# Performance work log

Measured on AMD Instinct MI355X. Metric: run time of the kernel, lower is better.

Reference implementation:

```python
import jax, jax.numpy as jnp
import numpy as np

N = 10000   # nodes (cells)
E = 100000  # edges
G = 2000    # num_genes
H = 20      # heads
C1 = 128    # layer-1 out channels per head
C2 = 128    # latent_dim
NEG_SLOPE = 0.2


def setup_inputs():
    key = jax.random.key(0)
    ks = jax.random.split(key, 9)
    s = 0.05
    return {
        "x": jax.random.normal(ks[0], (N, G), jnp.float32),
        "edge_index": jax.random.randint(ks[1], (2, E), 0, N, dtype=jnp.int64),
        "W1": jax.random.normal(ks[2], (G, H * C1), jnp.float32) * s,
        "att_src1": jax.random.normal(ks[3], (H, C1), jnp.float32) * s,
        "att_dst1": jax.random.normal(ks[4], (H, C1), jnp.float32) * s,
        "b1": jnp.zeros((H * C1,), jnp.float32),
        "W2": jax.random.normal(ks[5], (H * C1, H * C2), jnp.float32) * s,
        "att_src2": jax.random.normal(ks[6], (H, C2), jnp.float32) * s,
        "att_dst2": jax.random.normal(ks[7], (H, C2), jnp.float32) * s,
        "b2": jnp.zeros((C2,), jnp.float32),
    }


def _gat_conv(x, W, att_src, att_dst, bias, src, dst, concat):
    """PyG GATConv (eval mode, self-loops already in src/dst)."""
    n = x.shape[0]
    h_, c_ = att_src.shape
    h = (x @ W).reshape(n, h_, c_)                      # [N, H, C]
    a_src = jnp.einsum("nhc,hc->nh", h, att_src)        # [N, H]
    a_dst = jnp.einsum("nhc,hc->nh", h, att_dst)        # [N, H]
    e = a_src[src] + a_dst[dst]                          # [E, H]
    e = jnp.where(e > 0, e, NEG_SLOPE * e)               # leaky_relu
    # segment softmax over incoming edges of each destination node
    e_max = jax.ops.segment_max(e, dst, num_segments=n)  # [N, H]
    ex = jnp.exp(e - e_max[dst])                         # [E, H]
    denom = jax.ops.segment_sum(ex, dst, num_segments=n)
    alpha = ex / denom[dst]                              # [E, H]
    msg = alpha[:, :, None] * h[src]                     # [E, H, C]
    out = jax.ops.segment_sum(msg, dst, num_segments=n)  # [N, H, C]
    if concat:
        out = out.reshape(n, h_ * c_)
    else:
        out = out.mean(axis=1)                           # [N, C]
    return out + bias


def reference(x, edge_index, W1, att_src1, att_dst1, b1, W2, att_src2, att_dst2, b2):
    n = x.shape[0]
    loop = jnp.arange(n, dtype=edge_index.dtype)
    src = jnp.concatenate([edge_index[0], loop])  # PyG add_self_loops=True
    dst = jnp.concatenate([edge_index[1], loop])
    h1 = _gat_conv(x, W1, att_src1, att_dst1, b1, src, dst, concat=True)
    h1 = jax.nn.relu(h1)  # dropout is identity in eval mode
    h2 = _gat_conv(h1, W2, att_src2, att_dst2, b2, src, dst, concat=False)
    return jax.nn.relu(h2)
```

## Files before the change

### kernel.cpp

```cpp
#include <hip/hip_runtime.h>

#define NEG_SLOPE 0.2f

typedef __attribute__((ext_vector_type(4))) float floatx4;
typedef __attribute__((ext_vector_type(8))) short shortx8;

__device__ __forceinline__ unsigned short f2bf(float f) {
  union { float f; unsigned int u; } v;
  v.f = f;
  unsigned int r = (v.u + 0x7FFFu + ((v.u >> 16) & 1u)) >> 16;
  return (unsigned short)r;
}
__device__ __forceinline__ float bf2f(unsigned short u) {
  union { unsigned int u; float f; } v;
  v.u = (unsigned int)u << 16;
  return v.f;
}
__device__ __forceinline__ void store_out(float* p, float v) { *p = v; }
__device__ __forceinline__ void store_out(unsigned short* p, float v) { *p = f2bf(v); }

__device__ __forceinline__ void gload_lds16(const unsigned short* g, unsigned short* l) {
  __builtin_amdgcn_global_load_lds(
      (const __attribute__((address_space(1))) void*)(g),
      (__attribute__((address_space(3))) void*)(l), 16, 0, 0);
}

__device__ __forceinline__ int load_edge(const void* ei, long idx, int is64) {
  if (is64) return (int)((const long long*)ei)[idx];
  return ((const int*)ei)[idx];
}

__global__ void detect64_kernel(const unsigned int* __restrict__ p, int* __restrict__ flag) {
  int is64 = 1;
  for (int i = 0; i < 32; ++i)
    if (p[2 * i + 1] != 0u) is64 = 0;
  *flag = is64;
}

__global__ void init_cnt_kernel(int* __restrict__ cnt, int n) {
  int i = blockIdx.x * blockDim.x + threadIdx.x;
  if (i < n) cnt[i] = 1;
}

__global__ void count_kernel(const void* __restrict__ ei, const int* __restrict__ flag, int E,
                             int* __restrict__ cnt) {
  int e = blockIdx.x * blockDim.x + threadIdx.x;
  if (e >= E) return;
  int is64 = *flag;
  int d = load_edge(ei, (long)E + e, is64);
  atomicAdd(&cnt[d], 1);
}

__global__ __launch_bounds__(1024) void scan_kernel(const int* __restrict__ cnt,
                                                    int* __restrict__ offs, int n) {
  __shared__ int partial[1024];
  int t = threadIdx.x;
  int per = (n + 1023) / 1024;
  int beg = t * per;
  int end = min(beg + per, n);
  int sum = 0;
  for (int i = beg; i < end; ++i) sum += cnt[i];
  partial[t] = sum;
  __syncthreads();
  for (int d = 1; d < 1024; d <<= 1) {
    int v = (t >= d) ? partial[t - d] : 0;
    __syncthreads();
    partial[t] += v;
    __syncthreads();
  }
  int excl = (t == 0) ? 0 : partial[t - 1];
  for (int i = beg; i < end; ++i) { offs[i] = excl; excl += cnt[i]; }
  if (t == 1023) offs[n] = partial[1023];
}

__global__ void init_self_kernel(const int* __restrict__ offs, int* __restrict__ srcs,
                                 int* __restrict__ fill, int n) {
  int i = blockIdx.x * blockDim.x + threadIdx.x;
  if (i < n) { srcs[offs[i]] = i; fill[i] = 1; }
}

__global__ void scatter_kernel(const void* __restrict__ ei, const int* __restrict__ flag, int E,
                               const int* __restrict__ offs, int* __restrict__ fill,
                               int* __restrict__ srcs) {
  int e = blockIdx.x * blockDim.x + threadIdx.x;
  if (e >= E) return;
  int is64 = *flag;
  int s = load_edge(ei, e, is64);
  int d = load_edge(ei, (long)E + e, is64);
  int pos = offs[d] + atomicAdd(&fill[d], 1);
  srcs[pos] = s;
}


__global__ __launch_bounds__(256) void pack_a_kernel(const float* __restrict__ in,
                                                     unsigned short* __restrict__ out, int M,
                                                     int K, int Kpad) {
  int rt = blockIdx.x;
  int r = threadIdx.x & 127;
  int kq = threadIdx.x >> 7;
  int row = rt * 128 + r;
  int nkc = Kpad >> 3;
  unsigned short* obase = out + (long)rt * Kpad * 128 + r * 8;
  const float* irow = in + (long)row * K;
  for (int kc = kq + (int)blockIdx.y * 2; kc < nkc; kc += (int)gridDim.y * 2) {
    int k = kc << 3;
    shortx8 o;
    if (row < M && k + 8 <= K && (K & 3) == 0) {
      float4 v0 = *(const float4*)(irow + k);
      float4 v1 = *(const float4*)(irow + k + 4);
      o[0] = (short)f2bf(v0.x); o[1] = (short)f2bf(v0.y);
      o[2] = (short)f2bf(v0.z); o[3] = (short)f2bf(v0.w);
      o[4] = (short)f2bf(v1.x); o[5] = (short)f2bf(v1.y);
      o[6] = (short)f2bf(v1.z); o[7] = (short)f2bf(v1.w);
    } else {
#pragma unroll
      for (int i = 0; i < 8; ++i) {
        int kk = k + i;
        float v = (row < M && kk < K) ? irow[kk] : 0.f;
        o[i] = (short)f2bf(v);
      }
    }
    *(shortx8*)(obase + (long)kc * 1024) = o;
  }
}

__global__ __launch_bounds__(256) void transpose_pack_kernel(const float* __restrict__ in,
                                                             unsigned short* __restrict__ out,
                                                             int K, int N, int Kpad) {
  __shared__ float tile[32][33];
  int kb = blockIdx.x * 32;
  int nb = blockIdx.y * 32;
  int tx = threadIdx.x & 31;
  int ty = threadIdx.x >> 5;
#pragma unroll
  for (int i = 0; i < 32; i += 8) {
    int k = kb + ty + i;
    tile[ty + i][tx] = (k < K) ? in[(long)k * N + nb + tx] : 0.f;
  }
  __syncthreads();
  if (threadIdx.x < 128) {
    int nl = threadIdx.x & 31;
    int nn = nb + nl;
    int kc4 = threadIdx.x >> 5;
    int k0 = kc4 * 8;
    shortx8 o;
#pragma unroll
    for (int j = 0; j < 8; ++j) o[j] = (short)f2bf(tile[k0 + j][nl]);
    int kc = (kb >> 3) + kc4;
    *(shortx8*)(out + (long)(nn >> 7) * Kpad * 128 + (long)kc * 1024 + (nn & 127) * 8) = o;
  }
}

template <typename OT>
__global__ __launch_bounds__(256) void mfma_gemm_kernel(const unsigned short* __restrict__ A,
                                                        const unsigned short* __restrict__ Bt,
                                                        OT* __restrict__ C,
                                                        const float* __restrict__ att_s,
                                                        const float* __restrict__ att_d,
                                                        float* __restrict__ a_s,
                                                        float* __restrict__ a_d, int M, int N,
                                                        int K, int H) {
  __shared__ unsigned short As[3][4096];
  __shared__ unsigned short Bs[3][4096];
  __shared__ float red_s[2][128];
  __shared__ float red_d[2][128];

  int tid = threadIdx.x;
  int lane = tid & 63;
  int w = tid >> 6;
  int wm = w & 1, wn = w >> 1;
  int bn = blockIdx.x * 128;
  int bm = blockIdx.y * 128;
  int quad = lane >> 4, l16 = lane & 15;

  const unsigned short* pA = A + (long)(bm >> 7) * K * 128 + tid * 8;
  const unsigned short* pB = Bt + (long)(bn >> 7) * K * 128 + tid * 8;
  unsigned short* la = &As[0][0] + w * 512;
  unsigned short* lb = &Bs[0][0] + w * 512;

  floatx4 acc[4][4];
#pragma unroll
  for (int i = 0; i < 4; ++i)
#pragma unroll
    for (int j = 0; j < 4; ++j) acc[i][j] = (floatx4){0.f, 0.f, 0.f, 0.f};

  int nk = K >> 5;
  gload_lds16(pA, la);
  gload_lds16(pA + 2048, la + 2048);
  gload_lds16(pB, lb);
  gload_lds16(pB + 2048, lb + 2048);
  if (nk > 1) {
    gload_lds16(pA + 4096, la + 4096);
    gload_lds16(pA + 4096 + 2048, la + 4096 + 2048);
    gload_lds16(pB + 4096, lb + 4096);
    gload_lds16(pB + 4096 + 2048, lb + 4096 + 2048);
  }

  int cur = 0, st = 2;
  for (int k = 0; k < nk; ++k) {
    if (k + 2 < nk) {
      const unsigned short* qA = pA + (long)(k + 2) * 4096;
      const unsigned short* qB = pB + (long)(k + 2) * 4096;
      unsigned short* da = la + st * 4096;
      unsigned short* db = lb + st * 4096;
      gload_lds16(qA, da);
      gload_lds16(qA + 2048, da + 2048);
      gload_lds16(qB, db);
      gload_lds16(qB + 2048, db + 2048);
      __builtin_amdgcn_s_waitcnt(0x0F78);
    } else if (k + 1 < nk) {
      __builtin_amdgcn_s_waitcnt(0x0F74);
    } else {
      __builtin_amdgcn_s_waitcnt(0x0F70);
    }
    __builtin_amdgcn_s_barrier();

    shortx8 a[4], b[4];
#pragma unroll
    for (int i = 0; i < 4; ++i) {
      a[i] = *(const shortx8*)(&As[cur][(quad * 128 + wm * 64 + i * 16 + l16) * 8]);
      b[i] = *(const shortx8*)(&Bs[cur][(quad * 128 + wn * 64 + i * 16 + l16) * 8]);
    }
#pragma unroll
    for (int i = 0; i < 4; ++i)
#pragma unroll
      for (int j = 0; j < 4; ++j)
        acc[i][j] = __builtin_amdgcn_mfma_f32_16x16x32_bf16(a[i], b[j], acc[i][j], 0, 0, 0);

    __builtin_amdgcn_s_barrier();
    cur = (cur == 2) ? 0 : cur + 1;
    st = (st == 2) ? 0 : st + 1;
  }

  int hh = bn >> 7;
  float att_sv[4], att_dv[4];
#pragma unroll
  for (int j = 0; j < 4; ++j) {
    int cc = wn * 64 + j * 16 + l16;
    att_sv[j] = att_s[hh * 128 + cc];
    att_dv[j] = att_d[hh * 128 + cc];
  }
#pragma unroll
  for (int i = 0; i < 4; ++i)
#pragma unroll
    for (int r2 = 0; r2 < 4; ++r2) {
      float ps = 0.f, pd = 0.f;
#pragma unroll
      for (int j = 0; j < 4; ++j) {
        float v = acc[i][j][r2];
        ps = fmaf(v, att_sv[j], ps);
        pd = fmaf(v, att_dv[j], pd);
      }
#pragma unroll
      for (int msk = 1; msk < 16; msk <<= 1) {
        ps += __shfl_xor(ps, msk, 64);
        pd += __shfl_xor(pd, msk, 64);
      }
      if (l16 == 0) {
        int row = wm * 64 + quad * 4 + i * 16 + r2;
        red_s[wn][row] = ps;
        red_d[wn][row] = pd;
      }
    }

  int orow0 = bm + wm * 64 + quad * 4;
  int ocol0 = bn + wn * 64 + l16;
#pragma unroll
  for (int i = 0; i < 4; ++i)
#pragma unroll
    for (int j = 0; j < 4; ++j)
#pragma unroll
      for (int r2 = 0; r2 < 4; ++r2) {
        int rr = orow0 + i * 16 + r2;
        if (rr < M) store_out(&C[(long)rr * N + ocol0 + j * 16], acc[i][j][r2]);
      }

  __syncthreads();
  if (tid < 128) {
    int rr = bm + tid;
    if (rr < M) {
      a_s[(long)rr * H + hh] = red_s[0][tid] + red_s[1][tid];
      a_d[(long)rr * H + hh] = red_d[0][tid] + red_d[1][tid];
    }
  }
}

__global__ void edge_softmax_kernel(const float* __restrict__ a_src,
                                    const float* __restrict__ a_dst,
                                    const int* __restrict__ offs, const int* __restrict__ srcs,
                                    float* __restrict__ alpha, float* __restrict__ dinv, int n,
                                    int H) {
  int idx = blockIdx.x * blockDim.x + threadIdx.x;
  if (idx >= n * H) return;
  int dstn = idx / H;
  int hh = idx - dstn * H;
  int beg = offs[dstn], end = offs[dstn + 1];
  float ad = a_dst[idx];
  float m = -1e30f;
  for (int j = beg; j < end; ++j) {
    float e = a_src[srcs[j] * H + hh] + ad;
    e = e > 0.f ? e : NEG_SLOPE * e;
    alpha[(long)j * H + hh] = e;
    m = fmaxf(m, e);
  }
  float ssum = 0.f;
  for (int j = beg; j < end; ++j) {
    float ex = __expf(alpha[(long)j * H + hh] - m);
    alpha[(long)j * H + hh] = ex;
    ssum += ex;
  }
  dinv[idx] = 1.f / ssum;
}

__global__ __launch_bounds__(320) void aggregate1_kernel(const unsigned short* __restrict__ h,
                                                         const float* __restrict__ alpha,
                                                         const float* __restrict__ dinv,
                                                         const int* __restrict__ offs,
                                                         const int* __restrict__ srcs,
                                                         const float* __restrict__ bias,
                                                         unsigned short* __restrict__ out, int H,
                                                         int C, int HC, int Nn) {
  __shared__ unsigned short lds[8 * 2568];
  int t = threadIdx.x;
  int d0 = blockIdx.x * 8;
  int nf8 = HC >> 3;
  int fid = t;
  int hh = (fid << 3) / C;
  float bb[8];
#pragma unroll
  for (int i = 0; i < 8; ++i) bb[i] = bias[(fid << 3) + i];

  for (int ds = 0; ds < 8; ++ds) {
    int dst = d0 + ds;
    int beg = 0, end = 0;
    float di = 0.f;
    if (dst < Nn) {
      beg = offs[dst];
      end = offs[dst + 1];
      di = dinv[(long)dst * H + hh];
    }
    float acc[8];
#pragma unroll
    for (int i = 0; i < 8; ++i) acc[i] = 0.f;
    for (int j = beg; j < end; ++j) {
      int s = srcs[j];
      float al = alpha[(long)j * H + hh];
      shortx8 r = ((const shortx8*)(h + (long)s * HC))[fid];
#pragma unroll
      for (int i = 0; i < 8; ++i) acc[i] = fmaf(al, bf2f((unsigned short)r[i]), acc[i]);
    }
    shortx8 o;
#pragma unroll
    for (int i = 0; i < 8; ++i) o[i] = (short)f2bf(fmaxf(fmaf(acc[i], di, bb[i]), 0.f));
    *(shortx8*)&lds[ds * 2568 + fid * 8] = o;
  }
  __syncthreads();
  int sub = t & 7;
  int fg = t >> 3;
  int dst = d0 + sub;
  unsigned short* obase = out + (long)(dst >> 7) * HC * 128 + (dst & 127) * 8;
#pragma unroll
  for (int it = 0; it < 8; ++it) {
    int f = fg + 40 * it;
    shortx8 v = *(const shortx8*)&lds[sub * 2568 + f * 8];
    *(shortx8*)(obase + (long)f * 1024) = v;
  }
}

__global__ __launch_bounds__(256) void aggregate2_kernel(const unsigned short* __restrict__ h,
                                                         const float* __restrict__ alpha,
                                                         const float* __restrict__ dinv,
                                                         const int* __restrict__ offs,
                                                         const int* __restrict__ srcs,
                                                         const float* __restrict__ bias,
                                                         float* __restrict__ out, int H, int C) {
  __shared__ float smem[16 * 256];
  int dstn = blockIdx.x;
  int t = threadIdx.x;
  int HC = H * C;
  int nc8 = C >> 3;
  int c8 = t & (nc8 - 1);
  int hgrp = t >> __builtin_ctz(nc8);
  int nHgrp = 256 >> __builtin_ctz(nc8);
  int beg = offs[dstn], end = offs[dstn + 1];

  float acc[2][8];
#pragma unroll
  for (int hi = 0; hi < 2; ++hi)
#pragma unroll
    for (int i = 0; i < 8; ++i) acc[hi][i] = 0.f;

  for (int j = beg; j < end; ++j) {
    int s = srcs[j];
    const unsigned short* row = h + (long)s * HC;
    const float* al = alpha + (long)j * H;
#pragma unroll
    for (int hi = 0; hi < 2; ++hi) {
      int hh = hgrp + hi * nHgrp;
      if (hh < H) {
        float a = al[hh];
        shortx8 r = *(const shortx8*)(row + hh * C + c8 * 8);
#pragma unroll
        for (int i = 0; i < 8; ++i) acc[hi][i] = fmaf(a, bf2f((unsigned short)r[i]), acc[hi][i]);
      }
    }
  }
  float d0 = (hgrp < H) ? dinv[(long)dstn * H + hgrp] : 0.f;
  float d1 = (hgrp + nHgrp < H) ? dinv[(long)dstn * H + hgrp + nHgrp] : 0.f;
#pragma unroll
  for (int i = 0; i < 8; ++i)
    smem[hgrp * C + c8 * 8 + i] = acc[0][i] * d0 + acc[1][i] * d1;
  __syncthreads();
  float invH = 1.f / (float)H;
  for (int c = t; c < C; c += 256) {
    float s = 0.f;
    for (int g = 0; g < nHgrp; ++g) s += smem[g * C + c];
    float v = s * invH + bias[c];
    out[(long)dstn * C + c] = v > 0.f ? v : 0.f;
  }
}

static inline size_t align256(size_t x) { return (x + 255) & ~(size_t)255; }

extern "C" void kernel_launch(void* const* d_in, const int* in_sizes, int n_in, void* d_out,
                              int out_size, void* d_ws, size_t ws_size, hipStream_t stream) {
  const float* x        = (const float*)d_in[0];
  const void*  ei       = d_in[1];
  const float* W1       = (const float*)d_in[2];
  const float* att_src1 = (const float*)d_in[3];
  const float* att_dst1 = (const float*)d_in[4];
  const float* b1       = (const float*)d_in[5];
  const float* W2       = (const float*)d_in[6];
  const float* att_src2 = (const float*)d_in[7];
  const float* att_dst2 = (const float*)d_in[8];
  const float* b2       = (const float*)d_in[9];
  float* out = (float*)d_out;

  const int C2  = in_sizes[9];
  const int H   = in_sizes[7] / C2;
  const int HC1 = in_sizes[5];
  const int C1  = HC1 / H;
  const int G   = in_sizes[2] / HC1;
  const int Nn  = in_sizes[0] / G;
  const int E   = in_sizes[1] / 2;
  const int HC2 = H * C2;
  const int Et  = E + Nn;
  const int Mpad = ((Nn + 127) / 128) * 128;
  const int K1pad = ((G + 31) / 32) * 32;

  char* p = (char*)d_ws;
  size_t off = 0;
  unsigned short* hb  = (unsigned short*)(p + off); off = align256(off + (size_t)Mpad * (HC1 > HC2 ? HC1 : HC2) * 2);
  unsigned short* xb  = (unsigned short*)(p + off); off = align256(off + (size_t)Mpad * K1pad * 2);
  unsigned short* xb2 = (unsigned short*)(p + off); off = align256(off + (size_t)Mpad * HC1 * 2);
  unsigned short* W1t = (unsigned short*)(p + off); off = align256(off + (size_t)HC1 * K1pad * 2);
  unsigned short* W2t = (unsigned short*)(p + off); off = align256(off + (size_t)HC2 * HC1 * 2);
  float* a_s   = (float*)(p + off); off = align256(off + (size_t)Nn * H * 4);
  float* a_d   = (float*)(p + off); off = align256(off + (size_t)Nn * H * 4);
  float* dinv  = (float*)(p + off); off = align256(off + (size_t)Nn * H * 4);
  float* alpha = (float*)(p + off); off = align256(off + (size_t)Et * H * 4);
  int* cnt     = (int*)(p + off); off = align256(off + (size_t)Nn * 4);
  int* offs    = (int*)(p + off); off = align256(off + (size_t)(Nn + 1) * 4);
  int* fill    = (int*)(p + off); off = align256(off + (size_t)Nn * 4);
  int* srcs    = (int*)(p + off); off = align256(off + (size_t)Et * 4);
  int* flag64  = (int*)(p + off); off = align256(off + 16);
  (void)ws_size; (void)n_in; (void)out_size;

  const int TB = 256;
  detect64_kernel<<<1, 1, 0, stream>>>((const unsigned int*)ei, flag64);
  init_cnt_kernel<<<(Nn + TB - 1) / TB, TB, 0, stream>>>(cnt, Nn);
  count_kernel<<<(E + TB - 1) / TB, TB, 0, stream>>>(ei, flag64, E, cnt);
  scan_kernel<<<1, 1024, 0, stream>>>(cnt, offs, Nn);
  init_self_kernel<<<(Nn + TB - 1) / TB, TB, 0, stream>>>(offs, srcs, fill, Nn);
  scatter_kernel<<<(E + TB - 1) / TB, TB, 0, stream>>>(ei, flag64, E, offs, fill, srcs);

  {
    dim3 ga(Mpad / 128, 8);
    pack_a_kernel<<<ga, 256, 0, stream>>>(x, xb, Nn, G, K1pad);
    dim3 g1(K1pad / 32, HC1 / 32);
    transpose_pack_kernel<<<g1, 256, 0, stream>>>(W1, W1t, G, HC1, K1pad);
    dim3 g2(HC1 / 32, HC2 / 32);
    transpose_pack_kernel<<<g2, 256, 0, stream>>>(W2, W2t, HC1, HC2, HC1);
  }

  {
    dim3 grid(HC1 / 128, Mpad / 128);
    mfma_gemm_kernel<unsigned short><<<grid, 256, 0, stream>>>(xb, W1t, hb, att_src1, att_dst1,
                                                               a_s, a_d, Nn, HC1, K1pad, H);
  }
  edge_softmax_kernel<<<(Nn * H + TB - 1) / TB, TB, 0, stream>>>(a_s, a_d, offs, srcs, alpha, dinv, Nn, H);
  aggregate1_kernel<<<Mpad / 8, 320, 0, stream>>>(hb, alpha, dinv, offs, srcs, b1, xb2, H, C1, HC1, Nn);

  {
    dim3 grid(HC2 / 128, Mpad / 128);
    mfma_gemm_kernel<unsigned short><<<grid, 256, 0, stream>>>(xb2, W2t, hb, att_src2, att_dst2,
                                                               a_s, a_d, Nn, HC2, HC1, H);
  }
  edge_softmax_kernel<<<(Nn * H + TB - 1) / TB, TB, 0, stream>>>(a_s, a_d, offs, srcs, alpha, dinv, Nn, H);
  aggregate2_kernel<<<Nn, 256, 0, stream>>>(hb, alpha, dinv, offs, srcs, b2, out, H, C2);
}
```

Before: 783.9 us.

## Split layer-1 aggregation across feature chunks and 16 destinations per block

```diff
diff --git a/kernel.cpp b/kernel.cpp
--- a/kernel.cpp
+++ b/kernel.cpp
@@ -312,7 +312,7 @@
   dinv[idx] = 1.f / ssum;
 }
 
-__global__ __launch_bounds__(320) void aggregate1_kernel(const unsigned short* __restrict__ h,
+__global__ __launch_bounds__(256) void aggregate1_kernel(const unsigned short* __restrict__ h,
                                                          const float* __restrict__ alpha,
                                                          const float* __restrict__ dinv,
                                                          const int* __restrict__ offs,
@@ -320,51 +320,47 @@
                                                          const float* __restrict__ bias,
                                                          unsigned short* __restrict__ out, int H,
                                                          int C, int HC, int Nn) {
-  __shared__ unsigned short lds[8 * 2568];
+  __shared__ unsigned short lds[16 * 136];
   int t = threadIdx.x;
-  int d0 = blockIdx.x * 8;
-  int nf8 = HC >> 3;
-  int fid = t;
+  int cg = t & 15;
+  int sub = t >> 4;
+  int chunk = blockIdx.y;
+  int fid = chunk * 16 + cg;
+  int dst = blockIdx.x * 16 + sub;
   int hh = (fid << 3) / C;
   float bb[8];
 #pragma unroll
   for (int i = 0; i < 8; ++i) bb[i] = bias[(fid << 3) + i];
 
-  for (int ds = 0; ds < 8; ++ds) {
-    int dst = d0 + ds;
-    int beg = 0, end = 0;
-    float di = 0.f;
-    if (dst < Nn) {
-      beg = offs[dst];
-      end = offs[dst + 1];
-      di = dinv[(long)dst * H + hh];
-    }
-    float acc[8];
-#pragma unroll
-    for (int i = 0; i < 8; ++i) acc[i] = 0.f;
-    for (int j = beg; j < end; ++j) {
-      int s = srcs[j];
-      float al = alpha[(long)j * H + hh];
-      shortx8 r = ((const shortx8*)(h + (long)s * HC))[fid];
-#pragma unroll
-      for (int i = 0; i < 8; ++i) acc[i] = fmaf(al, bf2f((unsigned short)r[i]), acc[i]);
-    }
-    shortx8 o;
-#pragma unroll
-    for (int i = 0; i < 8; ++i) o[i] = (short)f2bf(fmaxf(fmaf(acc[i], di, bb[i]), 0.f));
-    *(shortx8*)&lds[ds * 2568 + fid * 8] = o;
-  }
+  int beg = 0, end = 0;
+  float di = 0.f;
+  if (dst < Nn) {
+    beg = offs[dst];
+    end = offs[dst + 1];
+    di = dinv[(long)dst * H + hh];
+  }
+  float acc[8];
+#pragma unroll
+  for (int i = 0; i < 8; ++i) acc[i] = 0.f;
+  const unsigned short* hsrc = h + (fid << 3);
+  for (int j = beg; j < end; ++j) {
+    int s = srcs[j];
+    float al = alpha[(long)j * H + hh];
+    shortx8 r = *(const shortx8*)(hsrc + (long)s * HC);
+#pragma unroll
+    for (int i = 0; i < 8; ++i) acc[i] = fmaf(al, bf2f((unsigned short)r[i]), acc[i]);
+  }
+  shortx8 o;
+#pragma unroll
+  for (int i = 0; i < 8; ++i) o[i] = (short)f2bf(fmaxf(fmaf(acc[i], di, bb[i]), 0.f));
+  *(shortx8*)&lds[sub * 136 + cg * 8] = o;
   __syncthreads();
-  int sub = t & 7;
-  int fg = t >> 3;
-  int dst = d0 + sub;
-  unsigned short* obase = out + (long)(dst >> 7) * HC * 128 + (dst & 127) * 8;
-#pragma unroll
-  for (int it = 0; it < 8; ++it) {
-    int f = fg + 40 * it;
-    shortx8 v = *(const shortx8*)&lds[sub * 2568 + f * 8];
-    *(shortx8*)(obase + (long)f * 1024) = v;
-  }
+  int sub2 = t & 15;
+  int fg = t >> 4;
+  int dst2 = blockIdx.x * 16 + sub2;
+  int fid2 = chunk * 16 + fg;
+  shortx8 v = *(const shortx8*)&lds[sub2 * 136 + fg * 8];
+  *(shortx8*)(out + (long)(dst2 >> 7) * HC * 128 + (long)fid2 * 1024 + (dst2 & 127) * 8) = v;
 }
 
 __global__ __launch_bounds__(256) void aggregate2_kernel(const unsigned short* __restrict__ h,
@@ -489,7 +485,10 @@
                                                                a_s, a_d, Nn, HC1, K1pad, H);
   }
   edge_softmax_kernel<<<(Nn * H + TB - 1) / TB, TB, 0, stream>>>(a_s, a_d, offs, srcs, alpha, dinv, Nn, H);
-  aggregate1_kernel<<<Mpad / 8, 320, 0, stream>>>(hb, alpha, dinv, offs, srcs, b1, xb2, H, C1, HC1, Nn);
+  {
+    dim3 ga1(Mpad / 16, HC1 / 128);
+    aggregate1_kernel<<<ga1, 256, 0, stream>>>(hb, alpha, dinv, offs, srcs, b1, xb2, H, C1, HC1, Nn);
+  }
 
   {
     dim3 grid(HC2 / 128, Mpad / 128);
```

Result: no change. 769.1 us (-1.9%).
